# Optimization experiments

Measured on AMD Instinct MI355X. Metric: run time of the kernel, lower is better.

Reference implementation:

```python
import jax, jax.numpy as jnp
import numpy as np

UNITS = 128

def setup_inputs() -> dict:
    key = jax.random.key(0)
    ks = jax.random.split(key, 8)
    B, Te, Td, De, Dd = 4, 512, 256, 512, 512
    enc = jax.random.normal(ks[0], (B, Te, De), dtype=jnp.float32)
    dec = jax.random.normal(ks[1], (B, Td, Dd), dtype=jnp.float32)
    # Dense params (glorot-ish scale)
    W1_w = jax.random.normal(ks[2], (De, UNITS), dtype=jnp.float32) / np.sqrt(De)
    W1_b = jnp.zeros((UNITS,), dtype=jnp.float32)
    W2_w = jax.random.normal(ks[3], (Dd, UNITS), dtype=jnp.float32) / np.sqrt(Dd)
    W2_b = jnp.zeros((UNITS,), dtype=jnp.float32)
    V_w = jax.random.normal(ks[4], (UNITS, 1), dtype=jnp.float32) / np.sqrt(UNITS)
    V_b = jnp.zeros((1,), dtype=jnp.float32)
    return {"encoder_out": enc, "decoder_out": dec,
            "W1_w": W1_w, "W1_b": W1_b, "W2_w": W2_w, "W2_b": W2_b,
            "V_w": V_w, "V_b": V_b}

def reference(encoder_out, decoder_out, W1_w, W1_b, W2_w, W2_b, V_w, V_b):
    # Project once per side (faithful: Dense is applied to broadcasted tensors,
    # but Dense commutes with broadcasting so projecting first is identical math).
    enc_p = jnp.einsum('bed,du->beu', encoder_out, W1_w) + W1_b   # [B,Te,U]
    dec_p = jnp.einsum('btd,du->btu', decoder_out, W2_w) + W2_b   # [B,Td,U]
    # Broadcast add -> tanh -> V score: [B,Td,Te]
    h = jnp.tanh(enc_p[:, None, :, :] + dec_p[:, :, None, :])     # [B,Td,Te,U]
    score = jnp.einsum('bteu,u->bte', h, V_w[:, 0]) + V_b[0]      # [B,Td,Te]
    attn_weights = jax.nn.softmax(score, axis=-1)
    context = jnp.einsum('bte,bed->btd', attn_weights, encoder_out)  # [B,Td,De]
    return (context, attn_weights)
```

## Files before the change

### kernel.cpp

```cpp
#include <hip/hip_runtime.h>

#define B  4
#define TE 512
#define TD 256
#define DE 512
#define U  128

#define RCPF(x)  __builtin_amdgcn_rcpf(x)
#define EXP2F(x) __builtin_amdgcn_exp2f(x)

#define ROWFMA(ar, xr) \
    ar.x += xr.x*w0.x + xr.y*w1.x + xr.z*w2.x + xr.w*w3.x; \
    ar.y += xr.x*w0.y + xr.y*w1.y + xr.z*w2.y + xr.w*w3.y; \
    ar.z += xr.x*w0.z + xr.y*w1.z + xr.z*w2.z + xr.w*w3.z; \
    ar.w += xr.x*w0.w + xr.y*w1.w + xr.z*w2.w + xr.w*w3.w;

#define ADD4(d, s) d.x += s.x; d.y += s.y; d.z += s.z; d.w += s.w;

__global__ __launch_bounds__(256) void proj_fused_kernel(
        const float* __restrict__ enc, const float* __restrict__ dec,
        const float* __restrict__ W1w, const float* __restrict__ W1b,
        const float* __restrict__ W2w, const float* __restrict__ W2b,
        float* __restrict__ encT, float* __restrict__ decp){
    __shared__ float4 Xs[8 * 128];
    __shared__ float4 Ps[3 * 4 * 64];
    float* T = (float*)Xs;
    const int tid = threadIdx.x;

    const bool is_enc = blockIdx.x < 256;
    const float *X, *W, *bias; int r0;
    if (is_enc){ r0 = blockIdx.x * 8;         X = enc; W = W1w; bias = W1b; }
    else       { r0 = (blockIdx.x - 256) * 8; X = dec; W = W2w; bias = W2b; }

    const float4* Xg = (const float4*)(X + (size_t)r0 * 512);
    #pragma unroll
    for (int j = 0; j < 4; ++j)
        Xs[j * 256 + tid] = Xg[j * 256 + tid];
    __syncthreads();

    const int q  = tid & 31;
    const int g  = (tid >> 5) & 1;
    const int ds = tid >> 6;
    const float4* W4 = (const float4*)W;

    float4 a0, a1, a2, a3;
    a0 = a1 = a2 = a3 = make_float4(0.f, 0.f, 0.f, 0.f);

    const int dbase = ds * 128;
    #pragma unroll 2
    for (int dd = 0; dd < 128; dd += 4){
        const int d0 = dbase + dd;
        const int xq = d0 >> 2;
        float4 x0 = Xs[(g + 0) * 128 + xq];
        float4 x1 = Xs[(g + 2) * 128 + xq];
        float4 x2 = Xs[(g + 4) * 128 + xq];
        float4 x3 = Xs[(g + 6) * 128 + xq];
        float4 w0 = W4[(d0 + 0) * 32 + q];
        float4 w1 = W4[(d0 + 1) * 32 + q];
        float4 w2 = W4[(d0 + 2) * 32 + q];
        float4 w3 = W4[(d0 + 3) * 32 + q];
        ROWFMA(a0, x0)
        ROWFMA(a1, x1)
        ROWFMA(a2, x2)
        ROWFMA(a3, x3)
    }

    const int slot = (g << 5) | q;
    if (ds){
        Ps[((ds-1)*4 + 0)*64 + slot] = a0;
        Ps[((ds-1)*4 + 1)*64 + slot] = a1;
        Ps[((ds-1)*4 + 2)*64 + slot] = a2;
        Ps[((ds-1)*4 + 3)*64 + slot] = a3;
    }
    __syncthreads();

    if (ds == 0){
        #pragma unroll
        for (int p = 0; p < 3; ++p){
            float4 r;
            r = Ps[(p*4 + 0)*64 + slot]; ADD4(a0, r)
            r = Ps[(p*4 + 1)*64 + slot]; ADD4(a1, r)
            r = Ps[(p*4 + 2)*64 + slot]; ADD4(a2, r)
            r = Ps[(p*4 + 3)*64 + slot]; ADD4(a3, r)
        }
        float4 bq = ((const float4*)bias)[q];
        ADD4(a0, bq) ADD4(a1, bq) ADD4(a2, bq) ADD4(a3, bq)

        const float C2 = 2.8853900817779268f;
        a0.x = EXP2F(a0.x*C2); a0.y = EXP2F(a0.y*C2); a0.z = EXP2F(a0.z*C2); a0.w = EXP2F(a0.w*C2);
        a1.x = EXP2F(a1.x*C2); a1.y = EXP2F(a1.y*C2); a1.z = EXP2F(a1.z*C2); a1.w = EXP2F(a1.w*C2);
        a2.x = EXP2F(a2.x*C2); a2.y = EXP2F(a2.y*C2); a2.z = EXP2F(a2.z*C2); a2.w = EXP2F(a2.w*C2);
        a3.x = EXP2F(a3.x*C2); a3.y = EXP2F(a3.y*C2); a3.z = EXP2F(a3.z*C2); a3.w = EXP2F(a3.w*C2);

        if (is_enc){
            T[(4*q+0)*9 + g + 0] = a0.x; T[(4*q+1)*9 + g + 0] = a0.y;
            T[(4*q+2)*9 + g + 0] = a0.z; T[(4*q+3)*9 + g + 0] = a0.w;
            T[(4*q+0)*9 + g + 2] = a1.x; T[(4*q+1)*9 + g + 2] = a1.y;
            T[(4*q+2)*9 + g + 2] = a1.z; T[(4*q+3)*9 + g + 2] = a1.w;
            T[(4*q+0)*9 + g + 4] = a2.x; T[(4*q+1)*9 + g + 4] = a2.y;
            T[(4*q+2)*9 + g + 4] = a2.z; T[(4*q+3)*9 + g + 4] = a2.w;
            T[(4*q+0)*9 + g + 6] = a3.x; T[(4*q+1)*9 + g + 6] = a3.y;
            T[(4*q+2)*9 + g + 6] = a3.z; T[(4*q+3)*9 + g + 6] = a3.w;
        } else {
            float4* D = (float4*)decp;
            D[(size_t)(r0 + g + 0) * 32 + q] = a0;
            D[(size_t)(r0 + g + 2) * 32 + q] = a1;
            D[(size_t)(r0 + g + 4) * 32 + q] = a2;
            D[(size_t)(r0 + g + 6) * 32 + q] = a3;
        }
    }
    __syncthreads();

    if (is_enc && tid < 128){
        const int u  = tid;
        const int bb = r0 >> 9;
        const int et = r0 & 511;
        float4 lo = make_float4(T[u*9+0], T[u*9+1], T[u*9+2], T[u*9+3]);
        float4 hi = make_float4(T[u*9+4], T[u*9+5], T[u*9+6], T[u*9+7]);
        float4* row = (float4*)encT + (size_t)(bb*U + u)*128 + (et >> 2);
        row[0] = lo; row[1] = hi;
    }
}

#define TANH_ACC(s, dv) \
    s.x += wv * RCPF(fmaf(A.x, dv, 1.0f)); \
    s.y += wv * RCPF(fmaf(A.y, dv, 1.0f)); \
    s.z += wv * RCPF(fmaf(A.z, dv, 1.0f)); \
    s.w += wv * RCPF(fmaf(A.w, dv, 1.0f));

__global__ __launch_bounds__(512) void score_kernel(
        const float* __restrict__ encT, const float* __restrict__ decp,
        const float* __restrict__ Vw, float* __restrict__ attn_out){
    __shared__ float4 dp4[128];
    __shared__ float4 vv4[32];
    __shared__ float4 Pp[3 * 4 * 128];
    __shared__ float redm[8], reds[8];
    const float* dpf = (const float*)dp4;
    const float* vvf = (const float*)vv4;
    const int tid = threadIdx.x;
    const int b  = blockIdx.x >> 6;
    const int t0 = (blockIdx.x & 63) * 4;

    if (tid < 128){
        dp4[tid] = ((const float4*)decp)[(size_t)(b*TD + t0 + (tid>>5))*32 + (tid&31)];
    } else if (tid < 160){
        float4 v = ((const float4*)Vw)[tid - 128];
        vv4[tid - 128] = make_float4(-2.f*v.x, -2.f*v.y, -2.f*v.z, -2.f*v.w);
    }
    __syncthreads();

    const int uh = tid >> 7;
    const int eq = tid & 127;
    const int u0 = uh * 32;

    const float4* E  = (const float4*)encT + (size_t)b*U*128 + (size_t)u0*128 + eq;
    const float* dt0 = dpf + 0*128 + u0;
    const float* dt1 = dpf + 1*128 + u0;
    const float* dt2 = dpf + 2*128 + u0;
    const float* dt3 = dpf + 3*128 + u0;
    const float* vv  = vvf + u0;

    float4 s0, s1, s2, s3;
    s0 = s1 = s2 = s3 = make_float4(0.f, 0.f, 0.f, 0.f);

    #pragma unroll 4
    for (int u = 0; u < 32; ++u){
        float4 A = E[(size_t)u * 128];
        float d0 = dt0[u], d1 = dt1[u], d2 = dt2[u], d3 = dt3[u];
        float wv = vv[u];
        TANH_ACC(s0, d0)
        TANH_ACC(s1, d1)
        TANH_ACC(s2, d2)
        TANH_ACC(s3, d3)
    }

    if (uh){
        Pp[((uh-1)*4 + 0)*128 + eq] = s0;
        Pp[((uh-1)*4 + 1)*128 + eq] = s1;
        Pp[((uh-1)*4 + 2)*128 + eq] = s2;
        Pp[((uh-1)*4 + 3)*128 + eq] = s3;
    }
    __syncthreads();

    float4 p0, p1, p2, p3;
    float m0, m1, m2, m3;
    const int w = tid >> 6;
    if (uh == 0){
        #pragma unroll
        for (int p = 0; p < 3; ++p){
            float4 r;
            r = Pp[(p*4 + 0)*128 + eq]; ADD4(s0, r)
            r = Pp[(p*4 + 1)*128 + eq]; ADD4(s1, r)
            r = Pp[(p*4 + 2)*128 + eq]; ADD4(s2, r)
            r = Pp[(p*4 + 3)*128 + eq]; ADD4(s3, r)
        }
        m0 = fmaxf(fmaxf(s0.x, s0.y), fmaxf(s0.z, s0.w));
        m1 = fmaxf(fmaxf(s1.x, s1.y), fmaxf(s1.z, s1.w));
        m2 = fmaxf(fmaxf(s2.x, s2.y), fmaxf(s2.z, s2.w));
        m3 = fmaxf(fmaxf(s3.x, s3.y), fmaxf(s3.z, s3.w));
        for (int o = 32; o > 0; o >>= 1){
            m0 = fmaxf(m0, __shfl_xor(m0, o));
            m1 = fmaxf(m1, __shfl_xor(m1, o));
            m2 = fmaxf(m2, __shfl_xor(m2, o));
            m3 = fmaxf(m3, __shfl_xor(m3, o));
        }
        if ((tid & 63) == 0){
            redm[0*2 + w] = m0; redm[1*2 + w] = m1;
            redm[2*2 + w] = m2; redm[3*2 + w] = m3;
        }
    }
    __syncthreads();
    if (uh == 0){
        m0 = fmaxf(redm[0], redm[1]); m1 = fmaxf(redm[2], redm[3]);
        m2 = fmaxf(redm[4], redm[5]); m3 = fmaxf(redm[6], redm[7]);
        const float L2E = 1.4426950408889634f;
        p0.x = EXP2F((s0.x-m0)*L2E); p0.y = EXP2F((s0.y-m0)*L2E);
        p0.z = EXP2F((s0.z-m0)*L2E); p0.w = EXP2F((s0.w-m0)*L2E);
        p1.x = EXP2F((s1.x-m1)*L2E); p1.y = EXP2F((s1.y-m1)*L2E);
        p1.z = EXP2F((s1.z-m1)*L2E); p1.w = EXP2F((s1.w-m1)*L2E);
        p2.x = EXP2F((s2.x-m2)*L2E); p2.y = EXP2F((s2.y-m2)*L2E);
        p2.z = EXP2F((s2.z-m2)*L2E); p2.w = EXP2F((s2.w-m2)*L2E);
        p3.x = EXP2F((s3.x-m3)*L2E); p3.y = EXP2F((s3.y-m3)*L2E);
        p3.z = EXP2F((s3.z-m3)*L2E); p3.w = EXP2F((s3.w-m3)*L2E);
        float l0 = (p0.x+p0.y)+(p0.z+p0.w);
        float l1 = (p1.x+p1.y)+(p1.z+p1.w);
        float l2 = (p2.x+p2.y)+(p2.z+p2.w);
        float l3 = (p3.x+p3.y)+(p3.z+p3.w);
        for (int o = 32; o > 0; o >>= 1){
            l0 += __shfl_xor(l0, o); l1 += __shfl_xor(l1, o);
            l2 += __shfl_xor(l2, o); l3 += __shfl_xor(l3, o);
        }
        if ((tid & 63) == 0){
            reds[0*2 + w] = l0; reds[1*2 + w] = l1;
            reds[2*2 + w] = l2; reds[3*2 + w] = l3;
        }
    }
    __syncthreads();
    if (uh == 0){
        float i0 = RCPF(reds[0] + reds[1]);
        float i1 = RCPF(reds[2] + reds[3]);
        float i2 = RCPF(reds[4] + reds[5]);
        float i3 = RCPF(reds[6] + reds[7]);
        float4* O = (float4*)attn_out;
        O[(size_t)(b*TD + t0 + 0)*128 + eq] = make_float4(p0.x*i0, p0.y*i0, p0.z*i0, p0.w*i0);
        O[(size_t)(b*TD + t0 + 1)*128 + eq] = make_float4(p1.x*i1, p1.y*i1, p1.z*i1, p1.w*i1);
        O[(size_t)(b*TD + t0 + 2)*128 + eq] = make_float4(p2.x*i2, p2.y*i2, p2.z*i2, p2.w*i2);
        O[(size_t)(b*TD + t0 + 3)*128 + eq] = make_float4(p3.x*i3, p3.y*i3, p3.z*i3, p3.w*i3);
    }
}

__global__ __launch_bounds__(512) void context_kernel(
        const float* __restrict__ enc, const float* __restrict__ attn,
        float* __restrict__ ctx_out){
    __shared__ float4 at4[8 * 128];
    __shared__ float4 red4[8 * 256];
    const int tid = threadIdx.x;
    const int dh = blockIdx.x & 1;
    const int b  = (blockIdx.x >> 1) & 3;
    const int t0 = (blockIdx.x >> 3) * 8;
    const int dq = tid & 63;
    const int eq = tid >> 6;

    const float4* A4 = (const float4*)(attn + (size_t)(b*TD + t0) * TE);
    at4[tid]       = A4[tid];
    at4[tid + 512] = A4[tid + 512];
    __syncthreads();

    float4 acc[8];
    #pragma unroll
    for (int t = 0; t < 8; ++t) acc[t] = make_float4(0.f, 0.f, 0.f, 0.f);

    const float4* eb = (const float4*)enc + (size_t)(b*TE)*128 + dh*64 + dq;
    for (int ec = 0; ec < 16; ++ec){
        const int e0 = eq*64 + ec*4;
        float4 x0 = eb[(size_t)(e0 + 0) * 128];
        float4 x1 = eb[(size_t)(e0 + 1) * 128];
        float4 x2 = eb[(size_t)(e0 + 2) * 128];
        float4 x3 = eb[(size_t)(e0 + 3) * 128];
        #pragma unroll
        for (int t = 0; t < 8; ++t){
            float4 w = at4[t*128 + (e0 >> 2)];
            acc[t].x += x0.x*w.x + x1.x*w.y + x2.x*w.z + x3.x*w.w;
            acc[t].y += x0.y*w.x + x1.y*w.y + x2.y*w.z + x3.y*w.w;
            acc[t].z += x0.z*w.x + x1.z*w.y + x2.z*w.z + x3.z*w.w;
            acc[t].w += x0.w*w.x + x1.w*w.y + x2.w*w.z + x3.w*w.w;
        }
    }

    for (int step = 4; step >= 1; step >>= 1){
        if (eq >= step && eq < 2*step){
            #pragma unroll
            for (int t = 0; t < 8; ++t)
                red4[t*256 + (eq - step)*64 + dq] = acc[t];
        }
        __syncthreads();
        if (eq < step){
            #pragma unroll
            for (int t = 0; t < 8; ++t){
                float4 r = red4[t*256 + eq*64 + dq];
                acc[t].x += r.x; acc[t].y += r.y; acc[t].z += r.z; acc[t].w += r.w;
            }
        }
        __syncthreads();
    }

    if (eq == 0){
        float4* ob = (float4*)ctx_out + (size_t)(b*TD + t0)*128 + dh*64 + dq;
        #pragma unroll
        for (int t = 0; t < 8; ++t) ob[t*128] = acc[t];
    }
}

extern "C" void kernel_launch(void* const* d_in, const int* in_sizes, int n_in,
                              void* d_out, int out_size, void* d_ws, size_t ws_size,
                              hipStream_t stream){
    const float* enc = (const float*)d_in[0];
    const float* dec = (const float*)d_in[1];
    const float* W1w = (const float*)d_in[2];
    const float* W1b = (const float*)d_in[3];
    const float* W2w = (const float*)d_in[4];
    const float* W2b = (const float*)d_in[5];
    const float* Vw  = (const float*)d_in[6];

    float* encT = (float*)d_ws;
    float* decp = encT + (size_t)B*U*TE;

    float* outp     = (float*)d_out;
    float* attn_out = outp + (size_t)B*TD*DE;

    hipLaunchKernelGGL(proj_fused_kernel, dim3(384), dim3(256), 0, stream,
                       enc, dec, W1w, W1b, W2w, W2b, encT, decp);
    hipLaunchKernelGGL(score_kernel, dim3(B*TD/4), dim3(512), 0, stream,
                       encT, decp, Vw, attn_out);
    hipLaunchKernelGGL(context_kernel, dim3(B*TD/8*2), dim3(512), 0, stream,
                       enc, attn_out, outp);
}
```

Before: 113.4 us.

## Fuse decoder projection into score kernel and widen encoder projection blocks

```diff
diff --git a/kernel.cpp b/kernel.cpp
--- a/kernel.cpp
+++ b/kernel.cpp
@@ -17,38 +17,31 @@
 
 #define ADD4(d, s) d.x += s.x; d.y += s.y; d.z += s.z; d.w += s.w;
 
-__global__ __launch_bounds__(256) void proj_fused_kernel(
-        const float* __restrict__ enc, const float* __restrict__ dec,
-        const float* __restrict__ W1w, const float* __restrict__ W1b,
-        const float* __restrict__ W2w, const float* __restrict__ W2b,
-        float* __restrict__ encT, float* __restrict__ decp){
+__global__ __launch_bounds__(512) void proj_enc_kernel(
+        const float* __restrict__ enc, const float* __restrict__ W1w,
+        const float* __restrict__ W1b, float* __restrict__ encT){
     __shared__ float4 Xs[8 * 128];
-    __shared__ float4 Ps[3 * 4 * 64];
+    __shared__ float4 Ps[7 * 8 * 32];
     float* T = (float*)Xs;
     const int tid = threadIdx.x;
-
-    const bool is_enc = blockIdx.x < 256;
-    const float *X, *W, *bias; int r0;
-    if (is_enc){ r0 = blockIdx.x * 8;         X = enc; W = W1w; bias = W1b; }
-    else       { r0 = (blockIdx.x - 256) * 8; X = dec; W = W2w; bias = W2b; }
-
-    const float4* Xg = (const float4*)(X + (size_t)r0 * 512);
-    #pragma unroll
-    for (int j = 0; j < 4; ++j)
-        Xs[j * 256 + tid] = Xg[j * 256 + tid];
+    const int r0 = blockIdx.x * 8;
+
+    const float4* Xg = (const float4*)(enc + (size_t)r0 * 512);
+    Xs[tid]       = Xg[tid];
+    Xs[tid + 512] = Xg[tid + 512];
     __syncthreads();
 
     const int q  = tid & 31;
     const int g  = (tid >> 5) & 1;
     const int ds = tid >> 6;
-    const float4* W4 = (const float4*)W;
+    const float4* W4 = (const float4*)W1w;
 
     float4 a0, a1, a2, a3;
     a0 = a1 = a2 = a3 = make_float4(0.f, 0.f, 0.f, 0.f);
 
-    const int dbase = ds * 128;
-    #pragma unroll 2
-    for (int dd = 0; dd < 128; dd += 4){
+    const int dbase = ds * 64;
+    #pragma unroll 4
+    for (int dd = 0; dd < 64; dd += 4){
         const int d0 = dbase + dd;
         const int xq = d0 >> 2;
         float4 x0 = Xs[(g + 0) * 128 + xq];
@@ -65,25 +58,24 @@
         ROWFMA(a3, x3)
     }
 
-    const int slot = (g << 5) | q;
     if (ds){
-        Ps[((ds-1)*4 + 0)*64 + slot] = a0;
-        Ps[((ds-1)*4 + 1)*64 + slot] = a1;
-        Ps[((ds-1)*4 + 2)*64 + slot] = a2;
-        Ps[((ds-1)*4 + 3)*64 + slot] = a3;
+        Ps[((ds-1)*8 + g + 0)*32 + q] = a0;
+        Ps[((ds-1)*8 + g + 2)*32 + q] = a1;
+        Ps[((ds-1)*8 + g + 4)*32 + q] = a2;
+        Ps[((ds-1)*8 + g + 6)*32 + q] = a3;
     }
     __syncthreads();
 
     if (ds == 0){
         #pragma unroll
-        for (int p = 0; p < 3; ++p){
+        for (int p = 0; p < 7; ++p){
             float4 r;
-            r = Ps[(p*4 + 0)*64 + slot]; ADD4(a0, r)
-            r = Ps[(p*4 + 1)*64 + slot]; ADD4(a1, r)
-            r = Ps[(p*4 + 2)*64 + slot]; ADD4(a2, r)
-            r = Ps[(p*4 + 3)*64 + slot]; ADD4(a3, r)
-        }
-        float4 bq = ((const float4*)bias)[q];
+            r = Ps[(p*8 + g + 0)*32 + q]; ADD4(a0, r)
+            r = Ps[(p*8 + g + 2)*32 + q]; ADD4(a1, r)
+            r = Ps[(p*8 + g + 4)*32 + q]; ADD4(a2, r)
+            r = Ps[(p*8 + g + 6)*32 + q]; ADD4(a3, r)
+        }
+        float4 bq = ((const float4*)W1b)[q];
         ADD4(a0, bq) ADD4(a1, bq) ADD4(a2, bq) ADD4(a3, bq)
 
         const float C2 = 2.8853900817779268f;
@@ -92,26 +84,18 @@
         a2.x = EXP2F(a2.x*C2); a2.y = EXP2F(a2.y*C2); a2.z = EXP2F(a2.z*C2); a2.w = EXP2F(a2.w*C2);
         a3.x = EXP2F(a3.x*C2); a3.y = EXP2F(a3.y*C2); a3.z = EXP2F(a3.z*C2); a3.w = EXP2F(a3.w*C2);
 
-        if (is_enc){
-            T[(4*q+0)*9 + g + 0] = a0.x; T[(4*q+1)*9 + g + 0] = a0.y;
-            T[(4*q+2)*9 + g + 0] = a0.z; T[(4*q+3)*9 + g + 0] = a0.w;
-            T[(4*q+0)*9 + g + 2] = a1.x; T[(4*q+1)*9 + g + 2] = a1.y;
-            T[(4*q+2)*9 + g + 2] = a1.z; T[(4*q+3)*9 + g + 2] = a1.w;
-            T[(4*q+0)*9 + g + 4] = a2.x; T[(4*q+1)*9 + g + 4] = a2.y;
-            T[(4*q+2)*9 + g + 4] = a2.z; T[(4*q+3)*9 + g + 4] = a2.w;
-            T[(4*q+0)*9 + g + 6] = a3.x; T[(4*q+1)*9 + g + 6] = a3.y;
-            T[(4*q+2)*9 + g + 6] = a3.z; T[(4*q+3)*9 + g + 6] = a3.w;
-        } else {
-            float4* D = (float4*)decp;
-            D[(size_t)(r0 + g + 0) * 32 + q] = a0;
-            D[(size_t)(r0 + g + 2) * 32 + q] = a1;
-            D[(size_t)(r0 + g + 4) * 32 + q] = a2;
-            D[(size_t)(r0 + g + 6) * 32 + q] = a3;
-        }
-    }
-    __syncthreads();
-
-    if (is_enc && tid < 128){
+        T[(4*q+0)*9 + g + 0] = a0.x; T[(4*q+1)*9 + g + 0] = a0.y;
+        T[(4*q+2)*9 + g + 0] = a0.z; T[(4*q+3)*9 + g + 0] = a0.w;
+        T[(4*q+0)*9 + g + 2] = a1.x; T[(4*q+1)*9 + g + 2] = a1.y;
+        T[(4*q+2)*9 + g + 2] = a1.z; T[(4*q+3)*9 + g + 2] = a1.w;
+        T[(4*q+0)*9 + g + 4] = a2.x; T[(4*q+1)*9 + g + 4] = a2.y;
+        T[(4*q+2)*9 + g + 4] = a2.z; T[(4*q+3)*9 + g + 4] = a2.w;
+        T[(4*q+0)*9 + g + 6] = a3.x; T[(4*q+1)*9 + g + 6] = a3.y;
+        T[(4*q+2)*9 + g + 6] = a3.z; T[(4*q+3)*9 + g + 6] = a3.w;
+    }
+    __syncthreads();
+
+    if (tid < 128){
         const int u  = tid;
         const int bb = r0 >> 9;
         const int et = r0 & 511;
@@ -129,8 +113,10 @@
     s.w += wv * RCPF(fmaf(A.w, dv, 1.0f));
 
 __global__ __launch_bounds__(512) void score_kernel(
-        const float* __restrict__ encT, const float* __restrict__ decp,
+        const float* __restrict__ encT, const float* __restrict__ dec,
+        const float* __restrict__ W2w, const float* __restrict__ W2b,
         const float* __restrict__ Vw, float* __restrict__ attn_out){
+    __shared__ float4 Xd[4 * 128];
     __shared__ float4 dp4[128];
     __shared__ float4 vv4[32];
     __shared__ float4 Pp[3 * 4 * 128];
@@ -141,13 +127,47 @@
     const int b  = blockIdx.x >> 6;
     const int t0 = (blockIdx.x & 63) * 4;
 
-    if (tid < 128){
-        dp4[tid] = ((const float4*)decp)[(size_t)(b*TD + t0 + (tid>>5))*32 + (tid&31)];
-    } else if (tid < 160){
-        float4 v = ((const float4*)Vw)[tid - 128];
-        vv4[tid - 128] = make_float4(-2.f*v.x, -2.f*v.y, -2.f*v.z, -2.f*v.w);
-    }
-    __syncthreads();
+    Xd[tid] = ((const float4*)dec)[(size_t)(b*TD + t0) * 128 + tid];
+    if (tid < 32){
+        float4 v = ((const float4*)Vw)[tid];
+        vv4[tid] = make_float4(-2.f*v.x, -2.f*v.y, -2.f*v.z, -2.f*v.w);
+    }
+    __syncthreads();
+
+    {
+        const int q  = tid & 31;
+        const int g  = (tid >> 5) & 3;
+        const int ds = tid >> 7;
+        const float4* W24 = (const float4*)W2w;
+        const float4* Xrow = Xd + g * 128;
+        float4 acc = make_float4(0.f, 0.f, 0.f, 0.f);
+        const int dbase = ds * 128;
+        #pragma unroll 2
+        for (int dd = 0; dd < 128; dd += 4){
+            const int d0 = dbase + dd;
+            float4 xr = Xrow[d0 >> 2];
+            float4 w0 = W24[(d0 + 0) * 32 + q];
+            float4 w1 = W24[(d0 + 1) * 32 + q];
+            float4 w2 = W24[(d0 + 2) * 32 + q];
+            float4 w3 = W24[(d0 + 3) * 32 + q];
+            ROWFMA(acc, xr)
+        }
+        if (ds) Pp[((ds-1)*4 + g)*32 + q] = acc;
+        __syncthreads();
+        if (ds == 0){
+            #pragma unroll
+            for (int p = 0; p < 3; ++p){
+                float4 r = Pp[(p*4 + g)*32 + q]; ADD4(acc, r)
+            }
+            float4 bq = ((const float4*)W2b)[q];
+            ADD4(acc, bq)
+            const float C2 = 2.8853900817779268f;
+            acc.x = EXP2F(acc.x*C2); acc.y = EXP2F(acc.y*C2);
+            acc.z = EXP2F(acc.z*C2); acc.w = EXP2F(acc.w*C2);
+            dp4[g*32 + q] = acc;
+        }
+        __syncthreads();
+    }
 
     const int uh = tid >> 7;
     const int eq = tid & 127;
@@ -323,15 +343,14 @@
     const float* Vw  = (const float*)d_in[6];
 
     float* encT = (float*)d_ws;
-    float* decp = encT + (size_t)B*U*TE;
 
     float* outp     = (float*)d_out;
     float* attn_out = outp + (size_t)B*TD*DE;
 
-    hipLaunchKernelGGL(proj_fused_kernel, dim3(384), dim3(256), 0, stream,
-                       enc, dec, W1w, W1b, W2w, W2b, encT, decp);
+    hipLaunchKernelGGL(proj_enc_kernel, dim3(B*TE/8), dim3(512), 0, stream,
+                       enc, W1w, W1b, encT);
     hipLaunchKernelGGL(score_kernel, dim3(B*TD/4), dim3(512), 0, stream,
-                       encT, decp, Vw, attn_out);
+                       encT, dec, W2w, W2b, Vw, attn_out);
     hipLaunchKernelGGL(context_kernel, dim3(B*TD/8*2), dim3(512), 0, stream,
                        enc, attn_out, outp);
 }
```

After: 116.4 us. 1.03x slower.

## Split decoder projection across more blocks and parallelize softmax across all warps

Applied to the files above, without the earlier changes.

```diff
diff --git a/kernel.cpp b/kernel.cpp
--- a/kernel.cpp
+++ b/kernel.cpp
@@ -26,11 +26,12 @@
     __shared__ float4 Ps[3 * 4 * 64];
     float* T = (float*)Xs;
     const int tid = threadIdx.x;
-
-    const bool is_enc = blockIdx.x < 256;
-    const float *X, *W, *bias; int r0;
-    if (is_enc){ r0 = blockIdx.x * 8;         X = enc; W = W1w; bias = W1b; }
-    else       { r0 = (blockIdx.x - 256) * 8; X = dec; W = W2w; bias = W2b; }
+    const int bid = blockIdx.x;
+    const bool is_enc = bid < 256;
+
+    const float* X; int r0; int uHalf = 0;
+    if (is_enc){ r0 = bid * 8; X = enc; }
+    else       { r0 = ((bid - 256) >> 1) * 8; uHalf = (bid - 256) & 1; X = dec; }
 
     const float4* Xg = (const float4*)(X + (size_t)r0 * 512);
     #pragma unroll
@@ -38,61 +39,62 @@
         Xs[j * 256 + tid] = Xg[j * 256 + tid];
     __syncthreads();
 
-    const int q  = tid & 31;
-    const int g  = (tid >> 5) & 1;
-    const int ds = tid >> 6;
-    const float4* W4 = (const float4*)W;
-
-    float4 a0, a1, a2, a3;
-    a0 = a1 = a2 = a3 = make_float4(0.f, 0.f, 0.f, 0.f);
-
-    const int dbase = ds * 128;
-    #pragma unroll 2
-    for (int dd = 0; dd < 128; dd += 4){
-        const int d0 = dbase + dd;
-        const int xq = d0 >> 2;
-        float4 x0 = Xs[(g + 0) * 128 + xq];
-        float4 x1 = Xs[(g + 2) * 128 + xq];
-        float4 x2 = Xs[(g + 4) * 128 + xq];
-        float4 x3 = Xs[(g + 6) * 128 + xq];
-        float4 w0 = W4[(d0 + 0) * 32 + q];
-        float4 w1 = W4[(d0 + 1) * 32 + q];
-        float4 w2 = W4[(d0 + 2) * 32 + q];
-        float4 w3 = W4[(d0 + 3) * 32 + q];
-        ROWFMA(a0, x0)
-        ROWFMA(a1, x1)
-        ROWFMA(a2, x2)
-        ROWFMA(a3, x3)
-    }
-
-    const int slot = (g << 5) | q;
-    if (ds){
-        Ps[((ds-1)*4 + 0)*64 + slot] = a0;
-        Ps[((ds-1)*4 + 1)*64 + slot] = a1;
-        Ps[((ds-1)*4 + 2)*64 + slot] = a2;
-        Ps[((ds-1)*4 + 3)*64 + slot] = a3;
-    }
-    __syncthreads();
-
-    if (ds == 0){
-        #pragma unroll
-        for (int p = 0; p < 3; ++p){
-            float4 r;
-            r = Ps[(p*4 + 0)*64 + slot]; ADD4(a0, r)
-            r = Ps[(p*4 + 1)*64 + slot]; ADD4(a1, r)
-            r = Ps[(p*4 + 2)*64 + slot]; ADD4(a2, r)
-            r = Ps[(p*4 + 3)*64 + slot]; ADD4(a3, r)
-        }
-        float4 bq = ((const float4*)bias)[q];
-        ADD4(a0, bq) ADD4(a1, bq) ADD4(a2, bq) ADD4(a3, bq)
-
-        const float C2 = 2.8853900817779268f;
-        a0.x = EXP2F(a0.x*C2); a0.y = EXP2F(a0.y*C2); a0.z = EXP2F(a0.z*C2); a0.w = EXP2F(a0.w*C2);
-        a1.x = EXP2F(a1.x*C2); a1.y = EXP2F(a1.y*C2); a1.z = EXP2F(a1.z*C2); a1.w = EXP2F(a1.w*C2);
-        a2.x = EXP2F(a2.x*C2); a2.y = EXP2F(a2.y*C2); a2.z = EXP2F(a2.z*C2); a2.w = EXP2F(a2.w*C2);
-        a3.x = EXP2F(a3.x*C2); a3.y = EXP2F(a3.y*C2); a3.z = EXP2F(a3.z*C2); a3.w = EXP2F(a3.w*C2);
-
-        if (is_enc){
+    const float C2 = 2.8853900817779268f;
+
+    if (is_enc){
+        const int q  = tid & 31;
+        const int g  = (tid >> 5) & 1;
+        const int ds = tid >> 6;
+        const float4* W4 = (const float4*)W1w;
+
+        float4 a0, a1, a2, a3;
+        a0 = a1 = a2 = a3 = make_float4(0.f, 0.f, 0.f, 0.f);
+
+        const int dbase = ds * 128;
+        #pragma unroll 2
+        for (int dd = 0; dd < 128; dd += 4){
+            const int d0 = dbase + dd;
+            const int xq = d0 >> 2;
+            float4 x0 = Xs[(g + 0) * 128 + xq];
+            float4 x1 = Xs[(g + 2) * 128 + xq];
+            float4 x2 = Xs[(g + 4) * 128 + xq];
+            float4 x3 = Xs[(g + 6) * 128 + xq];
+            float4 w0 = W4[(d0 + 0) * 32 + q];
+            float4 w1 = W4[(d0 + 1) * 32 + q];
+            float4 w2 = W4[(d0 + 2) * 32 + q];
+            float4 w3 = W4[(d0 + 3) * 32 + q];
+            ROWFMA(a0, x0)
+            ROWFMA(a1, x1)
+            ROWFMA(a2, x2)
+            ROWFMA(a3, x3)
+        }
+
+        const int slot = (g << 5) | q;
+        if (ds){
+            Ps[((ds-1)*4 + 0)*64 + slot] = a0;
+            Ps[((ds-1)*4 + 1)*64 + slot] = a1;
+            Ps[((ds-1)*4 + 2)*64 + slot] = a2;
+            Ps[((ds-1)*4 + 3)*64 + slot] = a3;
+        }
+        __syncthreads();
+
+        if (ds == 0){
+            #pragma unroll
+            for (int p = 0; p < 3; ++p){
+                float4 r;
+                r = Ps[(p*4 + 0)*64 + slot]; ADD4(a0, r)
+                r = Ps[(p*4 + 1)*64 + slot]; ADD4(a1, r)
+                r = Ps[(p*4 + 2)*64 + slot]; ADD4(a2, r)
+                r = Ps[(p*4 + 3)*64 + slot]; ADD4(a3, r)
+            }
+            float4 bq = ((const float4*)W1b)[q];
+            ADD4(a0, bq) ADD4(a1, bq) ADD4(a2, bq) ADD4(a3, bq)
+
+            a0.x = EXP2F(a0.x*C2); a0.y = EXP2F(a0.y*C2); a0.z = EXP2F(a0.z*C2); a0.w = EXP2F(a0.w*C2);
+            a1.x = EXP2F(a1.x*C2); a1.y = EXP2F(a1.y*C2); a1.z = EXP2F(a1.z*C2); a1.w = EXP2F(a1.w*C2);
+            a2.x = EXP2F(a2.x*C2); a2.y = EXP2F(a2.y*C2); a2.z = EXP2F(a2.z*C2); a2.w = EXP2F(a2.w*C2);
+            a3.x = EXP2F(a3.x*C2); a3.y = EXP2F(a3.y*C2); a3.z = EXP2F(a3.z*C2); a3.w = EXP2F(a3.w*C2);
+
             T[(4*q+0)*9 + g + 0] = a0.x; T[(4*q+1)*9 + g + 0] = a0.y;
             T[(4*q+2)*9 + g + 0] = a0.z; T[(4*q+3)*9 + g + 0] = a0.w;
             T[(4*q+0)*9 + g + 2] = a1.x; T[(4*q+1)*9 + g + 2] = a1.y;
@@ -101,24 +103,64 @@
             T[(4*q+2)*9 + g + 4] = a2.z; T[(4*q+3)*9 + g + 4] = a2.w;
             T[(4*q+0)*9 + g + 6] = a3.x; T[(4*q+1)*9 + g + 6] = a3.y;
             T[(4*q+2)*9 + g + 6] = a3.z; T[(4*q+3)*9 + g + 6] = a3.w;
-        } else {
+        }
+        __syncthreads();
+
+        if (tid < 128){
+            const int u  = tid;
+            const int bb = r0 >> 9;
+            const int et = r0 & 511;
+            float4 lo = make_float4(T[u*9+0], T[u*9+1], T[u*9+2], T[u*9+3]);
+            float4 hi = make_float4(T[u*9+4], T[u*9+5], T[u*9+6], T[u*9+7]);
+            float4* row = (float4*)encT + (size_t)(bb*U + u)*128 + (et >> 2);
+            row[0] = lo; row[1] = hi;
+        }
+    } else {
+        const int q16 = tid & 15;
+        const int gg  = (tid >> 4) & 3;
+        const int ds  = tid >> 6;
+        const int wq  = uHalf * 16 + q16;
+        const float4* W4 = (const float4*)W2w;
+
+        float4 a0 = make_float4(0.f, 0.f, 0.f, 0.f);
+        float4 a1 = make_float4(0.f, 0.f, 0.f, 0.f);
+
+        const int dbase = ds * 128;
+        #pragma unroll 2
+        for (int dd = 0; dd < 128; dd += 4){
+            const int d0 = dbase + dd;
+            const int xq = d0 >> 2;
+            float4 x0 = Xs[(gg + 0) * 128 + xq];
+            float4 x1 = Xs[(gg + 4) * 128 + xq];
+            float4 w0 = W4[(d0 + 0) * 32 + wq];
+            float4 w1 = W4[(d0 + 1) * 32 + wq];
+            float4 w2 = W4[(d0 + 2) * 32 + wq];
+            float4 w3 = W4[(d0 + 3) * 32 + wq];
+            ROWFMA(a0, x0)
+            ROWFMA(a1, x1)
+        }
+
+        if (ds){
+            Ps[((ds-1)*8 + gg    )*16 + q16] = a0;
+            Ps[((ds-1)*8 + gg + 4)*16 + q16] = a1;
+        }
+        __syncthreads();
+
+        if (ds == 0){
+            #pragma unroll
+            for (int p = 0; p < 3; ++p){
+                float4 r;
+                r = Ps[(p*8 + gg    )*16 + q16]; ADD4(a0, r)
+                r = Ps[(p*8 + gg + 4)*16 + q16]; ADD4(a1, r)
+            }
+            float4 bq = ((const float4*)W2b)[wq];
+            ADD4(a0, bq) ADD4(a1, bq)
+            a0.x = EXP2F(a0.x*C2); a0.y = EXP2F(a0.y*C2); a0.z = EXP2F(a0.z*C2); a0.w = EXP2F(a0.w*C2);
+            a1.x = EXP2F(a1.x*C2); a1.y = EXP2F(a1.y*C2); a1.z = EXP2F(a1.z*C2); a1.w = EXP2F(a1.w*C2);
             float4* D = (float4*)decp;
-            D[(size_t)(r0 + g + 0) * 32 + q] = a0;
-            D[(size_t)(r0 + g + 2) * 32 + q] = a1;
-            D[(size_t)(r0 + g + 4) * 32 + q] = a2;
-            D[(size_t)(r0 + g + 6) * 32 + q] = a3;
-        }
-    }
-    __syncthreads();
-
-    if (is_enc && tid < 128){
-        const int u  = tid;
-        const int bb = r0 >> 9;
-        const int et = r0 & 511;
-        float4 lo = make_float4(T[u*9+0], T[u*9+1], T[u*9+2], T[u*9+3]);
-        float4 hi = make_float4(T[u*9+4], T[u*9+5], T[u*9+6], T[u*9+7]);
-        float4* row = (float4*)encT + (size_t)(bb*U + u)*128 + (et >> 2);
-        row[0] = lo; row[1] = hi;
+            D[(size_t)(r0 + gg    ) * 32 + wq] = a0;
+            D[(size_t)(r0 + gg + 4) * 32 + wq] = a1;
+        }
     }
 }
 
@@ -133,7 +175,7 @@
         const float* __restrict__ Vw, float* __restrict__ attn_out){
     __shared__ float4 dp4[128];
     __shared__ float4 vv4[32];
-    __shared__ float4 Pp[3 * 4 * 128];
+    __shared__ float4 Pp[4 * 4 * 128];
     __shared__ float redm[8], reds[8];
     const float* dpf = (const float*)dp4;
     const float* vvf = (const float*)vv4;
@@ -174,79 +216,42 @@
         TANH_ACC(s3, d3)
     }
 
-    if (uh){
-        Pp[((uh-1)*4 + 0)*128 + eq] = s0;
-        Pp[((uh-1)*4 + 1)*128 + eq] = s1;
-        Pp[((uh-1)*4 + 2)*128 + eq] = s2;
-        Pp[((uh-1)*4 + 3)*128 + eq] = s3;
-    }
-    __syncthreads();
-
-    float4 p0, p1, p2, p3;
-    float m0, m1, m2, m3;
-    const int w = tid >> 6;
-    if (uh == 0){
-        #pragma unroll
-        for (int p = 0; p < 3; ++p){
-            float4 r;
-            r = Pp[(p*4 + 0)*128 + eq]; ADD4(s0, r)
-            r = Pp[(p*4 + 1)*128 + eq]; ADD4(s1, r)
-            r = Pp[(p*4 + 2)*128 + eq]; ADD4(s2, r)
-            r = Pp[(p*4 + 3)*128 + eq]; ADD4(s3, r)
-        }
-        m0 = fmaxf(fmaxf(s0.x, s0.y), fmaxf(s0.z, s0.w));
-        m1 = fmaxf(fmaxf(s1.x, s1.y), fmaxf(s1.z, s1.w));
-        m2 = fmaxf(fmaxf(s2.x, s2.y), fmaxf(s2.z, s2.w));
-        m3 = fmaxf(fmaxf(s3.x, s3.y), fmaxf(s3.z, s3.w));
-        for (int o = 32; o > 0; o >>= 1){
-            m0 = fmaxf(m0, __shfl_xor(m0, o));
-            m1 = fmaxf(m1, __shfl_xor(m1, o));
-            m2 = fmaxf(m2, __shfl_xor(m2, o));
-            m3 = fmaxf(m3, __shfl_xor(m3, o));
-        }
-        if ((tid & 63) == 0){
-            redm[0*2 + w] = m0; redm[1*2 + w] = m1;
-            redm[2*2 + w] = m2; redm[3*2 + w] = m3;
-        }
-    }
-    __syncthreads();
-    if (uh == 0){
-        m0 = fmaxf(redm[0], redm[1]); m1 = fmaxf(redm[2], redm[3]);
-        m2 = fmaxf(redm[4], redm[5]); m3 = fmaxf(redm[6], redm[7]);
-        const float L2E = 1.4426950408889634f;
-        p0.x = EXP2F((s0.x-m0)*L2E); p0.y = EXP2F((s0.y-m0)*L2E);
-        p0.z = EXP2F((s0.z-m0)*L2E); p0.w = EXP2F((s0.w-m0)*L2E);
-        p1.x = EXP2F((s1.x-m1)*L2E); p1.y = EXP2F((s1.y-m1)*L2E);
-        p1.z = EXP2F((s1.z-m1)*L2E); p1.w = EXP2F((s1.w-m1)*L2E);
-        p2.x = EXP2F((s2.x-m2)*L2E); p2.y = EXP2F((s2.y-m2)*L2E);
-        p2.z = EXP2F((s2.z-m2)*L2E); p2.w = EXP2F((s2.w-m2)*L2E);
-        p3.x = EXP2F((s3.x-m3)*L2E); p3.y = EXP2F((s3.y-m3)*L2E);
-        p3.z = EXP2F((s3.z-m3)*L2E); p3.w = EXP2F((s3.w-m3)*L2E);
-        float l0 = (p0.x+p0.y)+(p0.z+p0.w);
-        float l1 = (p1.x+p1.y)+(p1.z+p1.w);
-        float l2 = (p2.x+p2.y)+(p2.z+p2.w);
-        float l3 = (p3.x+p3.y)+(p3.z+p3.w);
-        for (int o = 32; o > 0; o >>= 1){
-            l0 += __shfl_xor(l0, o); l1 += __shfl_xor(l1, o);
-            l2 += __shfl_xor(l2, o); l3 += __shfl_xor(l3, o);
-        }
-        if ((tid & 63) == 0){
-            reds[0*2 + w] = l0; reds[1*2 + w] = l1;
-            reds[2*2 + w] = l2; reds[3*2 + w] = l3;
-        }
-    }
-    __syncthreads();
-    if (uh == 0){
-        float i0 = RCPF(reds[0] + reds[1]);
-        float i1 = RCPF(reds[2] + reds[3]);
-        float i2 = RCPF(reds[4] + reds[5]);
-        float i3 = RCPF(reds[6] + reds[7]);
-        float4* O = (float4*)attn_out;
-        O[(size_t)(b*TD + t0 + 0)*128 + eq] = make_float4(p0.x*i0, p0.y*i0, p0.z*i0, p0.w*i0);
-        O[(size_t)(b*TD + t0 + 1)*128 + eq] = make_float4(p1.x*i1, p1.y*i1, p1.z*i1, p1.w*i1);
-        O[(size_t)(b*TD + t0 + 2)*128 + eq] = make_float4(p2.x*i2, p2.y*i2, p2.z*i2, p2.w*i2);
-        O[(size_t)(b*TD + t0 + 3)*128 + eq] = make_float4(p3.x*i3, p3.y*i3, p3.z*i3, p3.w*i3);
-    }
+    Pp[(uh*4 + 0)*128 + eq] = s0;
+    Pp[(uh*4 + 1)*128 + eq] = s1;
+    Pp[(uh*4 + 2)*128 + eq] = s2;
+    Pp[(uh*4 + 3)*128 + eq] = s3;
+    __syncthreads();
+
+    const int t = uh;
+    float4 s = Pp[(0*4 + t)*128 + eq];
+    {
+        float4 r;
+        r = Pp[(1*4 + t)*128 + eq]; ADD4(s, r)
+        r = Pp[(2*4 + t)*128 + eq]; ADD4(s, r)
+        r = Pp[(3*4 + t)*128 + eq]; ADD4(s, r)
+    }
+
+    float m = fmaxf(fmaxf(s.x, s.y), fmaxf(s.z, s.w));
+    for (int o = 32; o > 0; o >>= 1) m = fmaxf(m, __shfl_xor(m, o));
+    const int half = (tid >> 6) & 1;
+    if ((tid & 63) == 0) redm[t*2 + half] = m;
+    __syncthreads();
+    m = fmaxf(redm[t*2], redm[t*2 + 1]);
+
+    const float L2E = 1.4426950408889634f;
+    float4 p;
+    p.x = EXP2F((s.x - m) * L2E);
+    p.y = EXP2F((s.y - m) * L2E);
+    p.z = EXP2F((s.z - m) * L2E);
+    p.w = EXP2F((s.w - m) * L2E);
+    float l = (p.x + p.y) + (p.z + p.w);
+    for (int o = 32; o > 0; o >>= 1) l += __shfl_xor(l, o);
+    if ((tid & 63) == 0) reds[t*2 + half] = l;
+    __syncthreads();
+    float inv = RCPF(reds[t*2] + reds[t*2 + 1]);
+
+    ((float4*)attn_out)[(size_t)(b*TD + t0 + t)*128 + eq] =
+        make_float4(p.x*inv, p.y*inv, p.z*inv, p.w*inv);
 }
 
 __global__ __launch_bounds__(512) void context_kernel(
@@ -328,7 +333,7 @@
     float* outp     = (float*)d_out;
     float* attn_out = outp + (size_t)B*TD*DE;
 
-    hipLaunchKernelGGL(proj_fused_kernel, dim3(384), dim3(256), 0, stream,
+    hipLaunchKernelGGL(proj_fused_kernel, dim3(512), dim3(256), 0, stream,
                        enc, dec, W1w, W1b, W2w, W2b, encT, decp);
     hipLaunchKernelGGL(score_kernel, dim3(B*TD/4), dim3(512), 0, stream,
                        encT, decp, Vw, attn_out);
```

After: 113.8 us. Within noise of the previous version (+0.4%).
